# Performance work log

Hardware: AMD Instinct MI355X
Metric: run time of the kernel (lower is better)

Reference implementation:

```python
import jax, jax.numpy as jnp
import numpy as np

B, TOPK, H, I, E = 128, 8, 2048, 1408, 16


def setup_inputs() -> dict:
    key = jax.random.key(0)
    ks = jax.random.split(key, 8)
    x = jax.random.normal(ks[0], (B, H), dtype=jnp.float32)
    expert_ids = jax.random.randint(ks[1], (B, TOPK), 0, E, dtype=jnp.int32)
    smooth_scales = jax.random.uniform(ks[2], (E, I), dtype=jnp.float32, minval=0.5, maxval=1.5)
    expert_scales = jax.random.uniform(ks[3], (B, TOPK), dtype=jnp.float32)
    expert_scales = expert_scales / jnp.sum(expert_scales, axis=-1, keepdims=True)
    x_active_mask = jnp.ones((B,), dtype=bool)
    # int8-valued quantized expert weights (stored int32 for portability)
    w1 = jax.random.randint(ks[4], (E, H, 2 * I), -127, 128, dtype=jnp.int32)
    w1_scale = jax.random.uniform(ks[5], (E, 2 * I), dtype=jnp.float32, minval=1e-3, maxval=1e-2)
    w2 = jax.random.randint(ks[6], (E, I, H), -127, 128, dtype=jnp.int32)
    w2_scale = jax.random.uniform(ks[7], (E, H), dtype=jnp.float32, minval=1e-3, maxval=1e-2)
    return {"x": x, "expert_ids": expert_ids, "smooth_scales": smooth_scales,
            "expert_scales": expert_scales, "x_active_mask": x_active_mask,
            "w1": w1, "w1_scale": w1_scale, "w2": w2, "w2_scale": w2_scale}


def reference(x, expert_ids, smooth_scales, expert_scales, x_active_mask,
              w1, w1_scale, w2, w2_scale):
    # --- dispatch: dynamic per-token int8 quantization of x ---
    sx = jnp.maximum(jnp.max(jnp.abs(x), axis=-1, keepdims=True), 1e-12) / 127.0  # [B,1]
    xq = jnp.round(jnp.clip(x / sx, -128.0, 127.0))  # int8 values, fp32 storage
    # --- grouped GEMM1 (dense-equivalent of per-expert grouped matmul) ---
    h = jnp.einsum('bh,ehf->bef', xq, w1.astype(jnp.float32))  # [B,E,2I] int32 accum
    h = h * sx[:, :, None] * w1_scale[None]  # dequant: x_scale * per-channel w_scale
    # --- SwiGLU activation ---
    gate, up = h[..., :I], h[..., I:]
    act = jax.nn.silu(gate) * up  # [B,E,I]
    # --- smooth + dynamic re-quantization for GEMM2 ---
    act = act * smooth_scales[None]  # [B,E,I]
    s2 = jnp.maximum(jnp.max(jnp.abs(act), axis=-1, keepdims=True), 1e-12) / 127.0  # [B,E,1]
    aq = jnp.round(jnp.clip(act / s2, -128.0, 127.0))
    # --- grouped GEMM2 + dequant ---
    o = jnp.einsum('bei,eih->beh', aq, w2.astype(jnp.float32))  # [B,E,H]
    o = o * s2 * w2_scale[None]
    # --- combine: weighted sum over routed experts (scatter expert_scales to one-hot) ---
    comb = jnp.zeros((x.shape[0], w1.shape[0]), dtype=x.dtype)
    comb = comb.at[jnp.arange(x.shape[0])[:, None], expert_ids].add(expert_scales)  # [B,E]
    y = jnp.einsum('beh,be->bh', o, comb)
    return y * x_active_mask[:, None].astype(y.dtype)
```

## Files before the change

### kernel.cpp

```cpp
#include <hip/hip_runtime.h>
#include <math.h>

#define NB 128
#define NTOPK 8
#define NH 2048
#define NI 1408
#define NE 16
#define NTWO_I 2816
#define RR 16
#define NCF 7
#define SLOTS_PER_E (NCF * RR)
#define MAXSLOTS (NE * SLOTS_PER_E)

typedef int v4i __attribute__((ext_vector_type(4)));

__device__ __forceinline__ int pack4(int a, int b, int c, int d) {
    return (a & 0xff) | ((b & 0xff) << 8) | ((c & 0xff) << 16) | (d << 24);
}

__global__ void k_quant_x(const float* __restrict__ x,
                          int* __restrict__ xq8d,
                          float* __restrict__ sxv) {
    int b = blockIdx.x;
    int t = threadIdx.x;
    const float* xr = x + (size_t)b * NH;
    float m = 0.0f;
    for (int j = t; j < NH; j += 256) m = fmaxf(m, fabsf(xr[j]));
    __shared__ float red[256];
    red[t] = m;
    __syncthreads();
    for (int s = 128; s > 0; s >>= 1) {
        if (t < s) red[t] = fmaxf(red[t], red[t + s]);
        __syncthreads();
    }
    float scale = fmaxf(red[0], 1e-12f) / 127.0f;
    if (t == 0) sxv[b] = scale;
    for (int g = t; g < NH / 4; g += 256) {
        int q[4];
#pragma unroll
        for (int u = 0; u < 4; ++u)
            q[u] = (int)rintf(fminf(fmaxf(xr[4 * g + u] / scale, -128.0f), 127.0f));
        xq8d[(size_t)b * (NH / 4) + g] = pack4(q[0], q[1], q[2], q[3]);
    }
}

__global__ void k_route(const int* __restrict__ expert_ids,
                        const float* __restrict__ expert_scales,
                        int* __restrict__ slot_b,
                        float* __restrict__ slot_w,
                        int* __restrict__ nce_arr) {
    __shared__ int cnt[NE];
    __shared__ int fill[NE];
    int t = threadIdx.x;
    if (t < NE) { cnt[t] = 0; fill[t] = 0; }
    __syncthreads();
    for (int p = t; p < NB * NTOPK; p += 256) atomicAdd(&cnt[expert_ids[p]], 1);
    __syncthreads();
    if (t < NE) {
        int c = (cnt[t] + RR - 1) / RR;
        nce_arr[t] = c < NCF ? c : NCF;
    }
    for (int s = t; s < MAXSLOTS; s += 256) {
        slot_b[s] = 0;
        slot_w[s] = 0.0f;
    }
    __syncthreads();
    for (int p = t; p < NB * NTOPK; p += 256) {
        int e = expert_ids[p];
        int pos = atomicAdd(&fill[e], 1);
        if (pos < SLOTS_PER_E) {
            slot_b[e * SLOTS_PER_E + pos] = p >> 3;
            slot_w[e * SLOTS_PER_E + pos] = expert_scales[p];
        }
    }
}

__global__ __launch_bounds__(256) void k_gemm1(
    const int* __restrict__ xq8d,
    const int* __restrict__ slot_b, const int* __restrict__ nce_arr,
    const int* __restrict__ w1, int* __restrict__ h) {
    int e = blockIdx.y;
    int nce = nce_arr[e];
    if (nce == 0) return;
    int t = threadIdx.x;
    int wave = t >> 6;
    int lane = t & 63;
    int lm = lane & 15;
    int kl = lane >> 4;
    int slot0 = e * SLOTS_PER_E;
    int colb = blockIdx.x * 64 + wave * 16;

    int rb[NCF];
#pragma unroll
    for (int q = 0; q < NCF; ++q)
        rb[q] = (q < nce) ? slot_b[slot0 + q * RR + lm] : 0;

    const int* wp = w1 + (size_t)e * NH * NTWO_I + (size_t)(kl * 16) * NTWO_I + colb + lm;

    v4i acc[NCF];
#pragma unroll
    for (int q = 0; q < NCF; ++q) acc[q] = (v4i){0, 0, 0, 0};

    for (int kb = 0; kb < NH / 64; ++kb) {
        int w[16];
#pragma unroll
        for (int j = 0; j < 16; ++j) w[j] = wp[(size_t)j * NTWO_I];
        v4i b = {pack4(w[0], w[1], w[2], w[3]),
                 pack4(w[4], w[5], w[6], w[7]),
                 pack4(w[8], w[9], w[10], w[11]),
                 pack4(w[12], w[13], w[14], w[15])};
#pragma unroll
        for (int q = 0; q < NCF; ++q) {
            if (q < nce) {
                v4i a = *(const v4i*)(xq8d + (size_t)rb[q] * (NH / 4) + kb * 16 + kl * 4);
                acc[q] = __builtin_amdgcn_mfma_i32_16x16x64_i8(a, b, acc[q], 0, 0, 0);
            }
        }
        wp += (size_t)64 * NTWO_I;
    }

#pragma unroll
    for (int q = 0; q < NCF; ++q) {
        if (q < nce) {
            int* hp = h + (size_t)(slot0 + q * RR) * NTWO_I + colb + lm;
#pragma unroll
            for (int r = 0; r < 4; ++r)
                hp[(size_t)(kl * 4 + r) * NTWO_I] = acc[q][r];
        }
    }
}

__global__ void k_act(const int* __restrict__ h, const float* __restrict__ sxv,
                      const int* __restrict__ slot_b, const int* __restrict__ nce_arr,
                      const float* __restrict__ w1_scale, const float* __restrict__ smooth,
                      int* __restrict__ aq8d, float* __restrict__ s2f) {
    int slot = blockIdx.x;
    int e = slot / SLOTS_PER_E;
    int within = slot - e * SLOTS_PER_E;
    if ((within >> 4) >= nce_arr[e]) return;
    int t = threadIdx.x;
    float sx = sxv[slot_b[slot]];
    const int* hr = h + (size_t)slot * NTWO_I;
    const float* w1s = w1_scale + (size_t)e * NTWO_I;
    const float* sm = smooth + (size_t)e * NI;

    float av[8];
    float m = 0.0f;
    int it = 0;
    for (int g = t; g < NI / 4; g += 256, ++it) {
#pragma unroll
        for (int u = 0; u < 4; ++u) {
            int j = 4 * g + u;
            float gt = (float)hr[j] * sx * w1s[j];
            float up = (float)hr[j + NI] * sx * w1s[j + NI];
            float a = (gt / (1.0f + expf(-gt))) * up * sm[j];
            av[it * 4 + u] = a;
            m = fmaxf(m, fabsf(a));
        }
    }
    __shared__ float red[256];
    red[t] = m;
    __syncthreads();
    for (int s = 128; s > 0; s >>= 1) {
        if (t < s) red[t] = fmaxf(red[t], red[t + s]);
        __syncthreads();
    }
    float s2 = fmaxf(red[0], 1e-12f) / 127.0f;
    if (t == 0) s2f[slot] = s2;
    it = 0;
    for (int g = t; g < NI / 4; g += 256, ++it) {
        int q[4];
#pragma unroll
        for (int u = 0; u < 4; ++u)
            q[u] = (int)rintf(fminf(fmaxf(av[it * 4 + u] / s2, -128.0f), 127.0f));
        aq8d[(size_t)slot * (NI / 4) + g] = pack4(q[0], q[1], q[2], q[3]);
    }
}

__global__ __launch_bounds__(256) void k_gemm2(
    const int* __restrict__ aq8d, const float* __restrict__ s2f,
    const int* __restrict__ slot_b, const float* __restrict__ slot_w,
    const int* __restrict__ nce_arr,
    const int* __restrict__ w2, const float* __restrict__ w2_scale,
    float* __restrict__ y) {
    int e = blockIdx.y;
    int nce = nce_arr[e];
    if (nce == 0) return;
    int t = threadIdx.x;
    int wave = t >> 6;
    int lane = t & 63;
    int lm = lane & 15;
    int kl = lane >> 4;
    int slot0 = e * SLOTS_PER_E;
    int colb = blockIdx.x * 64 + wave * 16;

    const int* wp = w2 + (size_t)e * NI * NH + (size_t)(kl * 16) * NH + colb + lm;

    v4i acc[NCF];
#pragma unroll
    for (int q = 0; q < NCF; ++q) acc[q] = (v4i){0, 0, 0, 0};

    for (int kb = 0; kb < NI / 64; ++kb) {
        int w[16];
#pragma unroll
        for (int j = 0; j < 16; ++j) w[j] = wp[(size_t)j * NH];
        v4i b = {pack4(w[0], w[1], w[2], w[3]),
                 pack4(w[4], w[5], w[6], w[7]),
                 pack4(w[8], w[9], w[10], w[11]),
                 pack4(w[12], w[13], w[14], w[15])};
#pragma unroll
        for (int q = 0; q < NCF; ++q) {
            if (q < nce) {
                v4i a = *(const v4i*)(aq8d + (size_t)(slot0 + q * RR + lm) * (NI / 4)
                                      + kb * 16 + kl * 4);
                acc[q] = __builtin_amdgcn_mfma_i32_16x16x64_i8(a, b, acc[q], 0, 0, 0);
            }
        }
        wp += (size_t)64 * NH;
    }

    float w2s = w2_scale[(size_t)e * NH + colb + lm];
#pragma unroll
    for (int q = 0; q < NCF; ++q) {
        if (q < nce) {
#pragma unroll
            for (int r = 0; r < 4; ++r) {
                int s = slot0 + q * RR + kl * 4 + r;
                float cf = s2f[s] * slot_w[s];
                if (cf != 0.0f)
                    atomicAdd(y + (size_t)slot_b[s] * NH + colb + lm,
                              (float)acc[q][r] * cf * w2s);
            }
        }
    }
}

extern "C" void kernel_launch(void* const* d_in, const int* in_sizes, int n_in,
                              void* d_out, int out_size, void* d_ws, size_t ws_size,
                              hipStream_t stream) {
    const float* x = (const float*)d_in[0];
    const int* expert_ids = (const int*)d_in[1];
    const float* smooth = (const float*)d_in[2];
    const float* expert_scales = (const float*)d_in[3];
    const int* w1 = (const int*)d_in[5];
    const float* w1_scale = (const float*)d_in[6];
    const int* w2 = (const int*)d_in[7];
    const float* w2_scale = (const float*)d_in[8];
    float* y = (float*)d_out;

    char* p = (char*)d_ws;
    int* xq8d = (int*)p;               p += (size_t)NB * (NH / 4) * 4;
    float* sxv = (float*)p;            p += NB * 4;
    int* slot_b = (int*)p;             p += MAXSLOTS * 4;
    float* slot_w = (float*)p;         p += MAXSLOTS * 4;
    int* nce_arr = (int*)p;            p += NE * 4;
    float* s2f = (float*)p;            p += MAXSLOTS * 4;
    int* h = (int*)p;                  p += (size_t)MAXSLOTS * NTWO_I * 4;
    int* aq8d = (int*)p;               p += (size_t)MAXSLOTS * (NI / 4) * 4;

    hipMemsetAsync(d_out, 0, (size_t)out_size * sizeof(float), stream);

    k_quant_x<<<NB, 256, 0, stream>>>(x, xq8d, sxv);
    k_route<<<1, 256, 0, stream>>>(expert_ids, expert_scales, slot_b, slot_w, nce_arr);
    dim3 g1(NTWO_I / 64, NE);
    k_gemm1<<<g1, 256, 0, stream>>>(xq8d, slot_b, nce_arr, w1, h);
    k_act<<<MAXSLOTS, 256, 0, stream>>>(h, sxv, slot_b, nce_arr, w1_scale, smooth,
                                        aq8d, s2f);
    dim3 g2(NH / 64, NE);
    k_gemm2<<<g2, 256, 0, stream>>>(aq8d, s2f, slot_b, slot_w, nce_arr,
                                    w2, w2_scale, y);
}
```

Measured before the change: 686.9 us.

## Split-K both expert GEMMs four ways and pre-gather activations into k-blocked layout

Both grouped GEMMs now split the K dimension across four blocks along grid z. GEMM1 partial sums are combined with integer atomics into a zeroed h buffer, and GEMM2 partials go through the existing float atomics into y. A new gather kernel copies quantized x rows per slot into a k-block-major layout, and the activation kernel writes its quantized output in the same layout, so MFMA operand loads become contiguous. The aim is more blocks in flight to pull in the weight stream, which the original grid of 44 or 32 column tiles times 16 experts could not do. In exchange it adds an extra memset of h, an extra kernel launch, and atomic traffic.

Result: slower. 701.4 us (+2.1%).

```diff
diff --git a/kernel.cpp b/kernel.cpp
--- a/kernel.cpp
+++ b/kernel.cpp
@@ -11,6 +11,8 @@
 #define NCF 7
 #define SLOTS_PER_E (NCF * RR)
 #define MAXSLOTS (NE * SLOTS_PER_E)
+#define KB1 (NH / 64)
+#define KB2 (NI / 64)
 
 typedef int v4i __attribute__((ext_vector_type(4)));
 
@@ -75,9 +77,21 @@
     }
 }
 
+__global__ void k_gather_x(const int* __restrict__ xq8d,
+                           const int* __restrict__ slot_b,
+                           int* __restrict__ xg) {
+    int slot = blockIdx.x;
+    int t = threadIdx.x;
+    int rb = slot_b[slot];
+    const int* src = xq8d + (size_t)rb * (NH / 4);
+#pragma unroll
+    for (int g = t; g < NH / 4; g += 256)
+        xg[((size_t)(g >> 4) * MAXSLOTS + slot) * 16 + (g & 15)] = src[g];
+}
+
 __global__ __launch_bounds__(256) void k_gemm1(
-    const int* __restrict__ xq8d,
-    const int* __restrict__ slot_b, const int* __restrict__ nce_arr,
+    const int* __restrict__ xg,
+    const int* __restrict__ nce_arr,
     const int* __restrict__ w1, int* __restrict__ h) {
     int e = blockIdx.y;
     int nce = nce_arr[e];
@@ -89,19 +103,17 @@
     int kl = lane >> 4;
     int slot0 = e * SLOTS_PER_E;
     int colb = blockIdx.x * 64 + wave * 16;
-
-    int rb[NCF];
-#pragma unroll
-    for (int q = 0; q < NCF; ++q)
-        rb[q] = (q < nce) ? slot_b[slot0 + q * RR + lm] : 0;
-
-    const int* wp = w1 + (size_t)e * NH * NTWO_I + (size_t)(kl * 16) * NTWO_I + colb + lm;
+    int kb0 = blockIdx.z * (KB1 / 4);
+
+    const int* wp = w1 + (size_t)e * NH * NTWO_I
+                  + (size_t)(kb0 * 64 + kl * 16) * NTWO_I + colb + lm;
+    const int* ap = xg + ((size_t)kb0 * MAXSLOTS + slot0 + lm) * 16 + kl * 4;
 
     v4i acc[NCF];
 #pragma unroll
     for (int q = 0; q < NCF; ++q) acc[q] = (v4i){0, 0, 0, 0};
 
-    for (int kb = 0; kb < NH / 64; ++kb) {
+    for (int kb = 0; kb < KB1 / 4; ++kb) {
         int w[16];
 #pragma unroll
         for (int j = 0; j < 16; ++j) w[j] = wp[(size_t)j * NTWO_I];
@@ -112,11 +124,12 @@
 #pragma unroll
         for (int q = 0; q < NCF; ++q) {
             if (q < nce) {
-                v4i a = *(const v4i*)(xq8d + (size_t)rb[q] * (NH / 4) + kb * 16 + kl * 4);
+                v4i a = *(const v4i*)(ap + (size_t)q * RR * 16);
                 acc[q] = __builtin_amdgcn_mfma_i32_16x16x64_i8(a, b, acc[q], 0, 0, 0);
             }
         }
         wp += (size_t)64 * NTWO_I;
+        ap += (size_t)MAXSLOTS * 16;
     }
 
 #pragma unroll
@@ -125,7 +138,7 @@
             int* hp = h + (size_t)(slot0 + q * RR) * NTWO_I + colb + lm;
 #pragma unroll
             for (int r = 0; r < 4; ++r)
-                hp[(size_t)(kl * 4 + r) * NTWO_I] = acc[q][r];
+                atomicAdd(hp + (size_t)(kl * 4 + r) * NTWO_I, acc[q][r]);
         }
     }
 }
@@ -133,7 +146,7 @@
 __global__ void k_act(const int* __restrict__ h, const float* __restrict__ sxv,
                       const int* __restrict__ slot_b, const int* __restrict__ nce_arr,
                       const float* __restrict__ w1_scale, const float* __restrict__ smooth,
-                      int* __restrict__ aq8d, float* __restrict__ s2f) {
+                      int* __restrict__ aqg, float* __restrict__ s2f) {
     int slot = blockIdx.x;
     int e = slot / SLOTS_PER_E;
     int within = slot - e * SLOTS_PER_E;
@@ -173,12 +186,13 @@
 #pragma unroll
         for (int u = 0; u < 4; ++u)
             q[u] = (int)rintf(fminf(fmaxf(av[it * 4 + u] / s2, -128.0f), 127.0f));
-        aq8d[(size_t)slot * (NI / 4) + g] = pack4(q[0], q[1], q[2], q[3]);
+        aqg[((size_t)(g >> 4) * MAXSLOTS + slot) * 16 + (g & 15)] =
+            pack4(q[0], q[1], q[2], q[3]);
     }
 }
 
 __global__ __launch_bounds__(256) void k_gemm2(
-    const int* __restrict__ aq8d, const float* __restrict__ s2f,
+    const int* __restrict__ aqg, const float* __restrict__ s2f,
     const int* __restrict__ slot_b, const float* __restrict__ slot_w,
     const int* __restrict__ nce_arr,
     const int* __restrict__ w2, const float* __restrict__ w2_scale,
@@ -193,14 +207,18 @@
     int kl = lane >> 4;
     int slot0 = e * SLOTS_PER_E;
     int colb = blockIdx.x * 64 + wave * 16;
-
-    const int* wp = w2 + (size_t)e * NI * NH + (size_t)(kl * 16) * NH + colb + lm;
+    int kb0 = (KB2 * blockIdx.z) / 4;
+    int kb1 = (KB2 * (blockIdx.z + 1)) / 4;
+
+    const int* wp = w2 + (size_t)e * NI * NH
+                  + (size_t)(kb0 * 64 + kl * 16) * NH + colb + lm;
+    const int* ap = aqg + ((size_t)kb0 * MAXSLOTS + slot0 + lm) * 16 + kl * 4;
 
     v4i acc[NCF];
 #pragma unroll
     for (int q = 0; q < NCF; ++q) acc[q] = (v4i){0, 0, 0, 0};
 
-    for (int kb = 0; kb < NI / 64; ++kb) {
+    for (int kb = kb0; kb < kb1; ++kb) {
         int w[16];
 #pragma unroll
         for (int j = 0; j < 16; ++j) w[j] = wp[(size_t)j * NH];
@@ -211,12 +229,12 @@
 #pragma unroll
         for (int q = 0; q < NCF; ++q) {
             if (q < nce) {
-                v4i a = *(const v4i*)(aq8d + (size_t)(slot0 + q * RR + lm) * (NI / 4)
-                                      + kb * 16 + kl * 4);
+                v4i a = *(const v4i*)(ap + (size_t)q * RR * 16);
                 acc[q] = __builtin_amdgcn_mfma_i32_16x16x64_i8(a, b, acc[q], 0, 0, 0);
             }
         }
         wp += (size_t)64 * NH;
+        ap += (size_t)MAXSLOTS * 16;
     }
 
     float w2s = w2_scale[(size_t)e * NH + colb + lm];
@@ -255,18 +273,21 @@
     float* slot_w = (float*)p;         p += MAXSLOTS * 4;
     int* nce_arr = (int*)p;            p += NE * 4;
     float* s2f = (float*)p;            p += MAXSLOTS * 4;
+    int* xg = (int*)p;                 p += (size_t)KB1 * MAXSLOTS * 64;
+    int* aqg = (int*)p;                p += (size_t)KB2 * MAXSLOTS * 64;
     int* h = (int*)p;                  p += (size_t)MAXSLOTS * NTWO_I * 4;
-    int* aq8d = (int*)p;               p += (size_t)MAXSLOTS * (NI / 4) * 4;
 
     hipMemsetAsync(d_out, 0, (size_t)out_size * sizeof(float), stream);
+    hipMemsetAsync(h, 0, (size_t)MAXSLOTS * NTWO_I * 4, stream);
 
     k_quant_x<<<NB, 256, 0, stream>>>(x, xq8d, sxv);
     k_route<<<1, 256, 0, stream>>>(expert_ids, expert_scales, slot_b, slot_w, nce_arr);
-    dim3 g1(NTWO_I / 64, NE);
-    k_gemm1<<<g1, 256, 0, stream>>>(xq8d, slot_b, nce_arr, w1, h);
+    k_gather_x<<<MAXSLOTS, 256, 0, stream>>>(xq8d, slot_b, xg);
+    dim3 g1(NTWO_I / 64, NE, 4);
+    k_gemm1<<<g1, 256, 0, stream>>>(xg, nce_arr, w1, h);
     k_act<<<MAXSLOTS, 256, 0, stream>>>(h, sxv, slot_b, nce_arr, w1_scale, smooth,
-                                        aq8d, s2f);
-    dim3 g2(NH / 64, NE);
-    k_gemm2<<<g2, 256, 0, stream>>>(aq8d, s2f, slot_b, slot_w, nce_arr,
+                                        aqg, s2f);
+    dim3 g2(NH / 64, NE, 4);
+    k_gemm2<<<g2, 256, 0, stream>>>(aqg, s2f, slot_b, slot_w, nce_arr,
                                     w2, w2_scale, y);
 }
```
